# Kernel tuning notes

Hardware: AMD Instinct MI355X
Metric: run time of the kernel (lower is better)

## Reference

```python
import jax, jax.numpy as jnp
import numpy as np

D_MODEL = 1024


def setup_inputs() -> dict:
    key = jax.random.key(0)
    ks = jax.random.split(key, 7)
    s = 1.0 / np.sqrt(D_MODEL)
    return {
        "x": jax.random.normal(ks[0], (4, 4096, D_MODEL), dtype=jnp.float32),
        "Wq": jax.random.normal(ks[1], (D_MODEL, D_MODEL), dtype=jnp.float32) * s,
        "bq": jax.random.normal(ks[2], (D_MODEL,), dtype=jnp.float32) * s,
        "Wk": jax.random.normal(ks[3], (D_MODEL, D_MODEL), dtype=jnp.float32) * s,
        "bk": jax.random.normal(ks[4], (D_MODEL,), dtype=jnp.float32) * s,
        "Wv": jax.random.normal(ks[5], (D_MODEL, D_MODEL), dtype=jnp.float32) * s,
        "bv": jax.random.normal(ks[6], (D_MODEL,), dtype=jnp.float32) * s,
    }


def reference(x, Wq, bq, Wk, bk, Wv, bv):
    # nn.Linear: y = x @ W.T + b
    Q = jnp.einsum("bsd,ed->bse", x, Wq) + bq  # [B,S,D]
    K = jnp.einsum("bsd,ed->bse", x, Wk) + bk
    V = jnp.einsum("bsd,ed->bse", x, Wv) + bv
    scale = 1.0 / jnp.sqrt(jnp.asarray(x.shape[-1], dtype=x.dtype))
    KV = jnp.einsum("bsd,bse->bde", K, V) * scale  # [B,D,D]
    E = jnp.einsum("bsd,bde->bse", Q, KV)  # [B,S,D]
    return E
```

## Files before the change

### kernel.cpp

```cpp
#include <hip/hip_runtime.h>
#include <hip/hip_fp16.h>


#define BATCH 4
#define SEQ   4096
#define DM    1024

typedef _Float16 h8 __attribute__((ext_vector_type(8)));
typedef _Float16 h4 __attribute__((ext_vector_type(4)));
typedef float    f4 __attribute__((ext_vector_type(4)));

__device__ inline void gload_lds16(const _Float16* g, _Float16* l) {
    __builtin_amdgcn_global_load_lds(
        (const __attribute__((address_space(1))) void*)g,
        (__attribute__((address_space(3))) void*)l,
        16, 0, 0);
}

__device__ inline int xcd_swz(int bid, int grid) {
    const int q = grid >> 3;
    return (bid & 7) * q + (bid >> 3);
}

template<bool WRITE_RM>
__global__ __launch_bounds__(256) void cvt_transpose(
    const float* __restrict__ src, _Float16* __restrict__ dstT,
    _Float16* __restrict__ dstRM, int R, int C)
{
    __shared__ float tile[64][65];
    const long zoff = (long)blockIdx.z * R * C;
    src += zoff; dstT += zoff;
    if (WRITE_RM) dstRM += zoff;
    const int r0 = blockIdx.y * 64;
    const int c0 = blockIdx.x * 64;
    const int t  = threadIdx.x;
    const int tr = t >> 4;
    const int tc = (t & 15) * 4;
    #pragma unroll
    for (int i = 0; i < 4; ++i) {
        const int r = tr + i * 16;
        f4 v = *(const f4*)&src[(long)(r0 + r) * C + c0 + tc];
        tile[r][tc + 0] = v.x; tile[r][tc + 1] = v.y;
        tile[r][tc + 2] = v.z; tile[r][tc + 3] = v.w;
        if (WRITE_RM) {
            h4 h = { (_Float16)v.x, (_Float16)v.y, (_Float16)v.z, (_Float16)v.w };
            *(h4*)&dstRM[(long)(r0 + r) * C + c0 + tc] = h;
        }
    }
    __syncthreads();
    #pragma unroll
    for (int i = 0; i < 4; ++i) {
        const int c = tr + i * 16;
        h4 h = { (_Float16)tile[tc + 0][c], (_Float16)tile[tc + 1][c],
                 (_Float16)tile[tc + 2][c], (_Float16)tile[tc + 3][c] };
        *(h4*)&dstT[(long)(c0 + c) * R + r0 + tc] = h;
    }
}

__global__ __launch_bounds__(256) void cvt_pair(
    const float* __restrict__ s0, _Float16* __restrict__ d0,
    const float* __restrict__ s1, _Float16* __restrict__ d1)
{
    const int half = blockIdx.x >> 10;
    const long i = ((long)(blockIdx.x & 1023) * 256 + threadIdx.x) * 4;
    const float* s = half ? s1 : s0;
    _Float16*    d = half ? d1 : d0;
    f4 v = *(const f4*)(s + i);
    h4 h = { (_Float16)v.x, (_Float16)v.y, (_Float16)v.z, (_Float16)v.w };
    *(h4*)(d + i) = h;
}

__global__ __launch_bounds__(256) void rowsum_xt(
    const _Float16* __restrict__ xt, float* __restrict__ xs)
{
    const int gw   = blockIdx.x * 4 + (threadIdx.x >> 6);
    const int lane = threadIdx.x & 63;
    const _Float16* row = xt + (long)gw * SEQ;
    float s = 0.f;
    #pragma unroll
    for (int i = 0; i < SEQ; i += 512) {
        h8 v = *(const h8*)&row[i + lane * 8];
        #pragma unroll
        for (int j = 0; j < 8; ++j) s += (float)v[j];
    }
    #pragma unroll
    for (int off = 32; off; off >>= 1) s += __shfl_down(s, off);
    if (lane == 0) xs[gw] = s;
}

__global__ __launch_bounds__(256) void gemv_dual(
    const _Float16* __restrict__ Wvh, const _Float16* __restrict__ Wkh,
    const float* __restrict__ xs, const float* __restrict__ bv,
    float* __restrict__ dst)
{
    const int gw   = blockIdx.x * 4 + (threadIdx.x >> 6);
    const int half = gw >> 12;
    const int g    = gw & 4095;
    const int b    = g >> 10;
    const int o    = g & 1023;
    const int lane = threadIdx.x & 63;
    const _Float16* wr = (half ? Wkh : Wvh) + (long)o * 1024;
    const float*    v  = xs + b * 1024;
    float s = 0.f;
    #pragma unroll
    for (int i = 0; i < 2; ++i) {
        const int k = i * 512 + lane * 8;
        h8 wv = *(const h8*)&wr[k];
        f4 v0 = *(const f4*)&v[k];
        f4 v1 = *(const f4*)&v[k + 4];
        s += (float)wv[0] * v0.x + (float)wv[1] * v0.y +
             (float)wv[2] * v0.z + (float)wv[3] * v0.w +
             (float)wv[4] * v1.x + (float)wv[5] * v1.y +
             (float)wv[6] * v1.z + (float)wv[7] * v1.w;
    }
    #pragma unroll
    for (int off = 32; off; off >>= 1) s += __shfl_down(s, off);
    if (lane == 0) dst[gw] = s + (half ? 0.f : (float)SEQ * bv[o]);
}

__global__ __launch_bounds__(256) void gemv_k1024(
    const _Float16* __restrict__ W, long wZ,
    const float* __restrict__ vec, float* __restrict__ out)
{
    const int gw   = blockIdx.x * 4 + (threadIdx.x >> 6);
    const int b    = gw >> 10;
    const int o    = gw & 1023;
    const int lane = threadIdx.x & 63;
    const _Float16* wr = W + b * wZ + (long)o * 1024;
    float s = 0.f;
    #pragma unroll
    for (int i = 0; i < 2; ++i) {
        const int k = i * 512 + lane * 8;
        h8 wv = *(const h8*)&wr[k];
        f4 v0 = *(const f4*)&vec[k];
        f4 v1 = *(const f4*)&vec[k + 4];
        s += (float)wv[0] * v0.x + (float)wv[1] * v0.y +
             (float)wv[2] * v0.z + (float)wv[3] * v0.w +
             (float)wv[4] * v1.x + (float)wv[5] * v1.y +
             (float)wv[6] * v1.z + (float)wv[7] * v1.w;
    }
    #pragma unroll
    for (int off = 32; off; off >>= 1) s += __shfl_down(s, off);
    if (lane == 0) out[gw] = s;
}

__global__ __launch_bounds__(256) void reduce_gh(
    const _Float16* __restrict__ parts, _Float16* __restrict__ Gh)
{
    const long DD_ = (long)DM * DM;
    const long i = ((long)blockIdx.x * 256 + threadIdx.x) * 8;
    const long b = i >> 20;
    const long r = i & (DD_ - 1);
    const _Float16* p = parts + b * 4 * DD_ + r;
    h8 v0 = *(const h8*)&p[0];
    h8 v1 = *(const h8*)&p[DD_];
    h8 v2 = *(const h8*)&p[2 * DD_];
    h8 v3 = *(const h8*)&p[3 * DD_];
    h8 o;
    #pragma unroll
    for (int j = 0; j < 8; ++j) {
        float s = (float)v0[j] + (float)v1[j] + (float)v2[j] + (float)v3[j];
        o[j] = (_Float16)(s * 0.03125f);
    }
    *(h8*)&Gh[i] = o;
}

template<typename OutT, int BIAS>
__global__ __launch_bounds__(512, 1) void gemm8p(
    const _Float16* __restrict__ A, const _Float16* __restrict__ B,
    OutT* __restrict__ C,
    int K, int lda, int ldb, int ldc, int tilesX, int perZ,
    long aZ, long bZ, long cZ, int sk, long aK, long bK,
    const float* __restrict__ bc1, long bc1Z, float alpha)
{
    __shared__ _Float16 lds[2 * 32768];

    const int L  = xcd_swz(blockIdx.x, gridDim.x);
    const int z  = L / perZ;
    const int r0 = L - z * perZ;
    const int zb = z / sk;
    const int zk = z - zb * sk;
    A += (long)zb * aZ + (long)zk * aK;
    B += (long)zb * bZ + (long)zk * bK;
    C += (long)z * cZ;
    const float* pc1 = (BIAS == 1) ? bc1 + (long)zb * bc1Z : nullptr;

    const int tileM = (r0 / tilesX) * 256;
    const int tileN = (r0 % tilesX) * 256;
    const int tid   = threadIdx.x;
    const int lane  = tid & 63;
    const int wave  = tid >> 6;
    const int wr    = wave >> 2;
    const int wc    = wave & 3;
    const int la    = lane & 15;
    const int kg    = lane >> 4;

    auto stageA = [&](int buf, int mq, int kt) {
        _Float16* dst = &lds[buf * 32768 + mq * 8192];
        const int k0 = kt * 64;
        #pragma unroll
        for (int i = 0; i < 2; ++i) {
            const int U = i * 512 + tid;
            const int R = U >> 3, s = U & 7;
            const int gr = tileM + (R >> 6) * 128 + mq * 64 + (R & 63);
            gload_lds16(&A[(long)gr * lda + k0 + ((s ^ (R & 7)) << 3)], dst + U * 8);
        }
    };
    auto stageB = [&](int buf, int nq, int kt) {
        _Float16* dst = &lds[buf * 32768 + 16384 + nq * 8192];
        const int k0 = kt * 64;
        #pragma unroll
        for (int i = 0; i < 2; ++i) {
            const int U = i * 512 + tid;
            const int R = U >> 3, s = U & 7;
            const int gn = tileN + (R >> 5) * 64 + nq * 32 + (R & 31);
            gload_lds16(&B[(long)gn * ldb + k0 + ((s ^ (R & 7)) << 3)], dst + U * 8);
        }
    };

    f4 acc[8][4] = {};
    h8 af[4][2];
    h8 bf[2][2][2];

    auto readA = [&](int buf, int mq) {
        const _Float16* Ab = &lds[buf * 32768 + mq * 8192];
        #pragma unroll
        for (int mi = 0; mi < 4; ++mi)
            #pragma unroll
            for (int kk = 0; kk < 2; ++kk) {
                const int R = wr * 64 + mi * 16 + la;
                const int s = kk * 4 + kg;
                af[mi][kk] = *(const h8*)&Ab[R * 64 + ((s ^ (R & 7)) << 3)];
            }
    };
    auto readB = [&](int buf, int nq) {
        const _Float16* Bb = &lds[buf * 32768 + 16384 + nq * 8192];
        #pragma unroll
        for (int ni = 0; ni < 2; ++ni)
            #pragma unroll
            for (int kk = 0; kk < 2; ++kk) {
                const int R = wc * 32 + ni * 16 + la;
                const int s = kk * 4 + kg;
                bf[nq][ni][kk] = *(const h8*)&Bb[R * 64 + ((s ^ (R & 7)) << 3)];
            }
    };
    auto mfmaQ = [&](int mq, int nq) {
        __builtin_amdgcn_s_setprio(1);
        #pragma unroll
        for (int mi = 0; mi < 4; ++mi)
            #pragma unroll
            for (int ni = 0; ni < 2; ++ni)
                #pragma unroll
                for (int kk = 0; kk < 2; ++kk)
                    acc[mq * 4 + mi][nq * 2 + ni] =
                        __builtin_amdgcn_mfma_f32_16x16x32_f16(
                            af[mi][kk], bf[nq][ni][kk],
                            acc[mq * 4 + mi][nq * 2 + ni], 0, 0, 0);
        __builtin_amdgcn_s_setprio(0);
    };

    const int NT = K >> 6;

    stageA(0, 0, 0); stageA(0, 1, 0); stageB(0, 0, 0); stageB(0, 1, 0);
    if (NT > 1) {
        stageA(1, 0, 1); stageB(1, 0, 1);
        asm volatile("s_waitcnt vmcnt(4)" ::: "memory");
    } else {
        asm volatile("s_waitcnt vmcnt(0)" ::: "memory");
    }
    __builtin_amdgcn_sched_barrier(0);
    __builtin_amdgcn_s_barrier();

    for (int j = 0; j < NT; ++j) {
        const int buf = j & 1;
        readA(buf, 0); readB(buf, 0);
        if (j + 1 < NT) stageA(buf ^ 1, 1, j + 1);
        __builtin_amdgcn_s_barrier();
        mfmaQ(0, 0);
        __builtin_amdgcn_s_barrier();
        readB(buf, 1);
        if (j + 1 < NT) stageB(buf ^ 1, 1, j + 1);
        __builtin_amdgcn_s_barrier();
        mfmaQ(0, 1);
        __builtin_amdgcn_s_barrier();
        readA(buf, 1);
        if (j + 2 < NT) stageA(buf, 0, j + 2);
        __builtin_amdgcn_s_barrier();
        mfmaQ(1, 0);
        __builtin_amdgcn_s_barrier();
        if (j + 2 < NT) stageB(buf, 0, j + 2);
        __builtin_amdgcn_s_barrier();
        mfmaQ(1, 1);
        if (j + 2 < NT) {
            asm volatile("s_waitcnt vmcnt(4)" ::: "memory");
        } else if (j + 1 < NT) {
            asm volatile("s_waitcnt vmcnt(0)" ::: "memory");
        }
        __builtin_amdgcn_sched_barrier(0);
        __builtin_amdgcn_s_barrier();
    }

    #pragma unroll
    for (int mf = 0; mf < 8; ++mf) {
        #pragma unroll
        for (int nf = 0; nf < 4; ++nf) {
            const int col = tileN + wc * 64 + nf * 16 + la;
            #pragma unroll
            for (int jj = 0; jj < 4; ++jj) {
                const int row = tileM + wr * 128 + mf * 16 + kg * 4 + jj;
                float v = acc[mf][nf][jj] * alpha;
                if (BIAS == 1) v += pc1[col];
                C[(long)row * ldc + col] = (OutT)v;
            }
        }
    }
}

template<int BIAS>
__global__ __launch_bounds__(256) void gemm64(
    const _Float16* __restrict__ A, const _Float16* __restrict__ B,
    _Float16* __restrict__ C,
    int K, int lda, int ldb, int ldc, int tilesX, int perZ,
    long aZ, long bZ, long cZ,
    const float* __restrict__ bc1, long bc1Z,
    const float* __restrict__ br1, long br1Z,
    const float* __restrict__ bc2, long bc2Z,
    const float* __restrict__ br2, long br2Z,
    float beta)
{
    __shared__ _Float16 As[64 * 64];
    __shared__ _Float16 Bs[64 * 64];

    const int L  = xcd_swz(blockIdx.x, gridDim.x);
    const int z  = L / perZ;
    const int r0 = L - z * perZ;
    A += (long)z * aZ;
    B += (long)z * bZ;
    C += (long)z * cZ;
    const float* pc1 = nullptr; const float* pr1 = nullptr;
    const float* pc2 = nullptr; const float* pr2 = nullptr;
    if (BIAS == 3) {
        pc1 = bc1 + (long)z * bc1Z; pr1 = br1 + (long)z * br1Z;
        pc2 = bc2 + (long)z * bc2Z; pr2 = br2 + (long)z * br2Z;
    }

    const int tileM = (r0 / tilesX) * 64;
    const int tileN = (r0 % tilesX) * 64;
    const int tid   = threadIdx.x;
    const int lane  = tid & 63;
    const int wave  = tid >> 6;
    const int wm    = (wave >> 1) * 32;
    const int wn    = (wave & 1) * 32;
    const int srow  = tid >> 3;
    const int sslot = tid & 7;

    f4 acc[2][2] = {};
    const int arow = lane & 15;
    const int kg   = lane >> 4;

    for (int k0 = 0; k0 < K; k0 += 64) {
        #pragma unroll
        for (int i = 0; i < 2; ++i) {
            const int row   = i * 32 + srow;
            const int gslot = sslot ^ (row & 7);
            gload_lds16(&A[(long)(tileM + row) * lda + k0 + gslot * 8],
                        &As[row * 64 + sslot * 8]);
            gload_lds16(&B[(long)(tileN + row) * ldb + k0 + gslot * 8],
                        &Bs[row * 64 + sslot * 8]);
        }
        __syncthreads();

        #pragma unroll
        for (int kk = 0; kk < 64; kk += 32) {
            h8 af[2], bf[2];
            #pragma unroll
            for (int m = 0; m < 2; ++m) {
                const int rr   = wm + m * 16 + arow;
                const int slot = (kk >> 3) + kg;
                af[m] = *(const h8*)&As[rr * 64 + ((slot ^ (rr & 7)) << 3)];
            }
            #pragma unroll
            for (int n = 0; n < 2; ++n) {
                const int rr   = wn + n * 16 + arow;
                const int slot = (kk >> 3) + kg;
                bf[n] = *(const h8*)&Bs[rr * 64 + ((slot ^ (rr & 7)) << 3)];
            }
            #pragma unroll
            for (int m = 0; m < 2; ++m)
                #pragma unroll
                for (int n = 0; n < 2; ++n)
                    acc[m][n] = __builtin_amdgcn_mfma_f32_16x16x32_f16(
                        af[m], bf[n], acc[m][n], 0, 0, 0);
        }
        __syncthreads();
    }

    #pragma unroll
    for (int m = 0; m < 2; ++m) {
        #pragma unroll
        for (int n = 0; n < 2; ++n) {
            const int col = tileN + wn + n * 16 + arow;
            #pragma unroll
            for (int j = 0; j < 4; ++j) {
                const int row = tileM + wm + m * 16 + (lane >> 4) * 4 + j;
                float v = acc[m][n][j];
                if (BIAS == 3) v += beta * (pc1[col] * pr1[row] + pc2[col] * pr2[row]);
                C[(long)row * ldc + col] = (_Float16)v;
            }
        }
    }
}

extern "C" void kernel_launch(void* const* d_in, const int* in_sizes, int n_in,
                              void* d_out, int out_size, void* d_ws, size_t ws_size,
                              hipStream_t stream)
{
    const float* x  = (const float*)d_in[0];
    const float* Wq = (const float*)d_in[1];
    const float* bq = (const float*)d_in[2];
    const float* Wk = (const float*)d_in[3];
    const float* bk = (const float*)d_in[4];
    const float* Wv = (const float*)d_in[5];
    const float* bv = (const float*)d_in[6];
    float* out = (float*)d_out;

    const long DD = (long)DM * DM;
    const long DS = (long)DM * SEQ;

    char* base = (char*)d_ws;
    _Float16* xh   = (_Float16*)base;
    _Float16* xt   = (_Float16*)(base + 32l * 1024 * 1024);
    _Float16* Gh   = xt;
    _Float16* Ph   = xt + 4l * 1024 * 1024;
    _Float16* KVth = xt + 8l * 1024 * 1024;
    _Float16* Rth  = xt + 12l * 1024 * 1024;
    _Float16* Wqt  = (_Float16*)(base + 64l * 1024 * 1024);
    _Float16* Wkh  = Wqt + DD;
    _Float16* Wvh  = Wkh + DD;
    float*    xs   = (float*)(Wvh + DD);
    float*    u2   = xs + 4 * 1024;
    float*    w    = u2 + 4 * 1024;
    float*    cv   = w + 4 * 1024;
    _Float16* parts = (_Float16*)d_out;

    cvt_transpose<true ><<<dim3(16, 64, 4), 256, 0, stream>>>(x,  xt,  xh, SEQ, DM);
    cvt_transpose<false><<<dim3(16, 16, 1), 256, 0, stream>>>(Wq, Wqt, nullptr, DM, DM);
    cvt_pair<<<2048, 256, 0, stream>>>(Wk, Wkh, Wv, Wvh);

    rowsum_xt<<<1024, 256, 0, stream>>>(xt, xs);

    gemv_dual<<<2048, 256, 0, stream>>>(Wvh, Wkh, xs, bv, u2);

    gemm8p<_Float16, 0><<<256, 512, 0, stream>>>(
        xt, xt, parts, 1024, SEQ, SEQ, DM, 4, 16,
        DS, DS, DD, 4, 1024, 1024, nullptr, 0, 1.0f);

    reduce_gh<<<2048, 256, 0, stream>>>(parts, Gh);

    gemm64<0><<<1024, 256, 0, stream>>>(
        Wvh, Gh, Ph, 1024, DM, DM, DM, 16, 256,
        0, DD, DD, nullptr, 0, nullptr, 0, nullptr, 0, nullptr, 0, 0.f);

    gemm64<3><<<1024, 256, 0, stream>>>(
        Ph, Wkh, KVth, 1024, DM, DM, DM, 16, 256,
        DD, 0, DD, bk, 0, u2, 1024, w, 1024, bv, 0, 0.03125f);

    gemv_k1024<<<1024, 256, 0, stream>>>(KVth, DD, bq, cv);

    gemm64<0><<<1024, 256, 0, stream>>>(
        KVth, Wqt, Rth, 1024, DM, DM, DM, 16, 256,
        DD, 0, DD, nullptr, 0, nullptr, 0, nullptr, 0, nullptr, 0, 0.f);

    gemm8p<float, 1><<<256, 512, 0, stream>>>(
        xh, Rth, out, 1024, DM, DM, DM, 4, 64,
        DS, DD, DS, 1, 0, 0, cv, 1024, 1.0f);
}
```

Before: 174.2 us.

## Restructure gemm8p main loop into double-buffered register fragments with deeper prefetch

Rewrites the 256x256 GEMM main loop to process two K-tiles per iteration. It ping-pongs A and B fragments between two register sets so that each LDS read overlaps the previous quadrant's MFMAs, and it keeps both LDS buffers fully prefetched with a vmcnt(6) wait. This aims to hide LDS read latency behind MFMA work. The cost is higher register pressure, and the loop assumes NT is even (clamped stage indices re-load the last tile).

```diff
diff --git a/kernel.cpp b/kernel.cpp
--- a/kernel.cpp
+++ b/kernel.cpp
@@ -173,7 +173,7 @@
     long aZ, long bZ, long cZ, int sk, long aK, long bK,
     const float* __restrict__ bc1, long bc1Z, float alpha)
 {
-    __shared__ _Float16 lds[2 * 32768];
+    __shared__ _Float16 lds[2][4][8192];
 
     const int L  = xcd_swz(blockIdx.x, gridDim.x);
     const int z  = L / perZ;
@@ -194,9 +194,10 @@
     const int wc    = wave & 3;
     const int la    = lane & 15;
     const int kg    = lane >> 4;
+    const int NT    = K >> 6;
 
     auto stageA = [&](int buf, int mq, int kt) {
-        _Float16* dst = &lds[buf * 32768 + mq * 8192];
+        _Float16* dst = &lds[buf][mq][0];
         const int k0 = kt * 64;
         #pragma unroll
         for (int i = 0; i < 2; ++i) {
@@ -207,7 +208,7 @@
         }
     };
     auto stageB = [&](int buf, int nq, int kt) {
-        _Float16* dst = &lds[buf * 32768 + 16384 + nq * 8192];
+        _Float16* dst = &lds[buf][2 + nq][0];
         const int k0 = kt * 64;
         #pragma unroll
         for (int i = 0; i < 2; ++i) {
@@ -219,32 +220,32 @@
     };
 
     f4 acc[8][4] = {};
-    h8 af[4][2];
-    h8 bf[2][2][2];
-
-    auto readA = [&](int buf, int mq) {
-        const _Float16* Ab = &lds[buf * 32768 + mq * 8192];
+    h8 aS0[4][2], aS1[4][2];
+    h8 bS0[2][2], bS1[2][2];
+
+    auto readA = [&](h8 (*dst)[2], int buf, int mq) {
+        const _Float16* Ab = &lds[buf][mq][0];
         #pragma unroll
         for (int mi = 0; mi < 4; ++mi)
             #pragma unroll
             for (int kk = 0; kk < 2; ++kk) {
                 const int R = wr * 64 + mi * 16 + la;
                 const int s = kk * 4 + kg;
-                af[mi][kk] = *(const h8*)&Ab[R * 64 + ((s ^ (R & 7)) << 3)];
+                dst[mi][kk] = *(const h8*)&Ab[R * 64 + ((s ^ (R & 7)) << 3)];
             }
     };
-    auto readB = [&](int buf, int nq) {
-        const _Float16* Bb = &lds[buf * 32768 + 16384 + nq * 8192];
+    auto readB = [&](h8 (*dst)[2], int buf, int nq) {
+        const _Float16* Bb = &lds[buf][2 + nq][0];
         #pragma unroll
         for (int ni = 0; ni < 2; ++ni)
             #pragma unroll
             for (int kk = 0; kk < 2; ++kk) {
                 const int R = wc * 32 + ni * 16 + la;
                 const int s = kk * 4 + kg;
-                bf[nq][ni][kk] = *(const h8*)&Bb[R * 64 + ((s ^ (R & 7)) << 3)];
+                dst[ni][kk] = *(const h8*)&Bb[R * 64 + ((s ^ (R & 7)) << 3)];
             }
     };
-    auto mfmaQ = [&](int mq, int nq) {
+    auto mfmaQ = [&](int mq, int nq, h8 (*Af)[2], h8 (*Bf)[2]) {
         __builtin_amdgcn_s_setprio(1);
         #pragma unroll
         for (int mi = 0; mi < 4; ++mi)
@@ -254,48 +255,68 @@
                 for (int kk = 0; kk < 2; ++kk)
                     acc[mq * 4 + mi][nq * 2 + ni] =
                         __builtin_amdgcn_mfma_f32_16x16x32_f16(
-                            af[mi][kk], bf[nq][ni][kk],
+                            Af[mi][kk], Bf[ni][kk],
                             acc[mq * 4 + mi][nq * 2 + ni], 0, 0, 0);
         __builtin_amdgcn_s_setprio(0);
     };
 
-    const int NT = K >> 6;
-
     stageA(0, 0, 0); stageA(0, 1, 0); stageB(0, 0, 0); stageB(0, 1, 0);
-    if (NT > 1) {
-        stageA(1, 0, 1); stageB(1, 0, 1);
-        asm volatile("s_waitcnt vmcnt(4)" ::: "memory");
-    } else {
-        asm volatile("s_waitcnt vmcnt(0)" ::: "memory");
-    }
+    stageA(1, 0, 1); stageA(1, 1, 1); stageB(1, 0, 1); stageB(1, 1, 1);
+    asm volatile("s_waitcnt vmcnt(8)" ::: "memory");
     __builtin_amdgcn_sched_barrier(0);
     __builtin_amdgcn_s_barrier();
-
-    for (int j = 0; j < NT; ++j) {
-        const int buf = j & 1;
-        readA(buf, 0); readB(buf, 0);
-        if (j + 1 < NT) stageA(buf ^ 1, 1, j + 1);
-        __builtin_amdgcn_s_barrier();
-        mfmaQ(0, 0);
-        __builtin_amdgcn_s_barrier();
-        readB(buf, 1);
-        if (j + 1 < NT) stageB(buf ^ 1, 1, j + 1);
-        __builtin_amdgcn_s_barrier();
-        mfmaQ(0, 1);
-        __builtin_amdgcn_s_barrier();
-        readA(buf, 1);
-        if (j + 2 < NT) stageA(buf, 0, j + 2);
-        __builtin_amdgcn_s_barrier();
-        mfmaQ(1, 0);
-        __builtin_amdgcn_s_barrier();
-        if (j + 2 < NT) stageB(buf, 0, j + 2);
-        __builtin_amdgcn_s_barrier();
-        mfmaQ(1, 1);
-        if (j + 2 < NT) {
-            asm volatile("s_waitcnt vmcnt(4)" ::: "memory");
-        } else if (j + 1 < NT) {
-            asm volatile("s_waitcnt vmcnt(0)" ::: "memory");
-        }
+    readA(aS0, 0, 0);
+    readB(bS0, 0, 0);
+    asm volatile("s_waitcnt lgkmcnt(0)" ::: "memory");
+    __builtin_amdgcn_sched_barrier(0);
+    __builtin_amdgcn_s_barrier();
+
+    for (int i = 0; i < NT / 2; ++i) {
+        const int t  = 2 * i;
+        const int t2 = (t + 2 < NT) ? t + 2 : NT - 1;
+        const int t3 = (t + 3 < NT) ? t + 3 : NT - 1;
+        readB(bS1, 0, 1);
+        stageA(0, 0, t2);
+        __builtin_amdgcn_s_barrier();
+        mfmaQ(0, 0, aS0, bS0);
+        __builtin_amdgcn_s_barrier();
+        readA(aS1, 0, 1);
+        stageB(0, 0, t2);
+        __builtin_amdgcn_s_barrier();
+        mfmaQ(0, 1, aS0, bS1);
+        __builtin_amdgcn_s_barrier();
+        readA(aS0, 1, 0);
+        stageB(0, 1, t2);
+        __builtin_amdgcn_s_barrier();
+        mfmaQ(1, 0, aS1, bS0);
+        __builtin_amdgcn_s_barrier();
+        readB(bS0, 1, 0);
+        stageA(0, 1, t2);
+        __builtin_amdgcn_s_barrier();
+        mfmaQ(1, 1, aS1, bS1);
+        asm volatile("s_waitcnt vmcnt(6)" ::: "memory");
+        __builtin_amdgcn_sched_barrier(0);
+        __builtin_amdgcn_s_barrier();
+        readB(bS1, 1, 1);
+        stageA(1, 0, t3);
+        __builtin_amdgcn_s_barrier();
+        mfmaQ(0, 0, aS0, bS0);
+        __builtin_amdgcn_s_barrier();
+        readA(aS1, 1, 1);
+        stageB(1, 0, t3);
+        __builtin_amdgcn_s_barrier();
+        mfmaQ(0, 1, aS0, bS1);
+        __builtin_amdgcn_s_barrier();
+        readA(aS0, 0, 0);
+        stageB(1, 1, t3);
+        __builtin_amdgcn_s_barrier();
+        mfmaQ(1, 0, aS1, bS0);
+        __builtin_amdgcn_s_barrier();
+        readB(bS0, 0, 0);
+        stageA(1, 1, t3);
+        __builtin_amdgcn_s_barrier();
+        mfmaQ(1, 1, aS1, bS1);
+        asm volatile("s_waitcnt vmcnt(6)" ::: "memory");
         __builtin_amdgcn_sched_barrier(0);
         __builtin_amdgcn_s_barrier();
     }
@@ -448,7 +469,6 @@
     cvt_pair<<<2048, 256, 0, stream>>>(Wk, Wkh, Wv, Wvh);
 
     rowsum_xt<<<1024, 256, 0, stream>>>(xt, xs);
-
     gemv_dual<<<2048, 256, 0, stream>>>(Wvh, Wkh, xs, bv, u2);
 
     gemm8p<_Float16, 0><<<256, 512, 0, stream>>>(
```

After: 196.8 us. +13.0%, slower.

## Reassociate weight products to drop one batched GEMM from the chain

Applied to the files above, without the earlier changes.

Precomputes the batch-independent product Wk·Wq (Mh) inside the same launch as the P = Wv·G GEMM. The separate KV GEMM and the KV·Wq GEMM are replaced by a single GEMM of P against Mh, with bias terms folded into extra GEMV vectors (qk, qw, sv, cv). Weight conversion kernels are merged into one launch, and LDS wait counts are made explicit around the MFMA phases of gemm8p. The aim is to remove one 1024³×4 GEMM and several launches, at the cost of extra GEMVs and a different fp16 rounding order.

```diff
diff --git a/kernel.cpp b/kernel.cpp
--- a/kernel.cpp
+++ b/kernel.cpp
@@ -22,85 +22,7 @@
     return (bid & 7) * q + (bid >> 3);
 }
 
-template<bool WRITE_RM>
-__global__ __launch_bounds__(256) void cvt_transpose(
-    const float* __restrict__ src, _Float16* __restrict__ dstT,
-    _Float16* __restrict__ dstRM, int R, int C)
-{
-    __shared__ float tile[64][65];
-    const long zoff = (long)blockIdx.z * R * C;
-    src += zoff; dstT += zoff;
-    if (WRITE_RM) dstRM += zoff;
-    const int r0 = blockIdx.y * 64;
-    const int c0 = blockIdx.x * 64;
-    const int t  = threadIdx.x;
-    const int tr = t >> 4;
-    const int tc = (t & 15) * 4;
-    #pragma unroll
-    for (int i = 0; i < 4; ++i) {
-        const int r = tr + i * 16;
-        f4 v = *(const f4*)&src[(long)(r0 + r) * C + c0 + tc];
-        tile[r][tc + 0] = v.x; tile[r][tc + 1] = v.y;
-        tile[r][tc + 2] = v.z; tile[r][tc + 3] = v.w;
-        if (WRITE_RM) {
-            h4 h = { (_Float16)v.x, (_Float16)v.y, (_Float16)v.z, (_Float16)v.w };
-            *(h4*)&dstRM[(long)(r0 + r) * C + c0 + tc] = h;
-        }
-    }
-    __syncthreads();
-    #pragma unroll
-    for (int i = 0; i < 4; ++i) {
-        const int c = tr + i * 16;
-        h4 h = { (_Float16)tile[tc + 0][c], (_Float16)tile[tc + 1][c],
-                 (_Float16)tile[tc + 2][c], (_Float16)tile[tc + 3][c] };
-        *(h4*)&dstT[(long)(c0 + c) * R + r0 + tc] = h;
-    }
-}
-
-__global__ __launch_bounds__(256) void cvt_pair(
-    const float* __restrict__ s0, _Float16* __restrict__ d0,
-    const float* __restrict__ s1, _Float16* __restrict__ d1)
-{
-    const int half = blockIdx.x >> 10;
-    const long i = ((long)(blockIdx.x & 1023) * 256 + threadIdx.x) * 4;
-    const float* s = half ? s1 : s0;
-    _Float16*    d = half ? d1 : d0;
-    f4 v = *(const f4*)(s + i);
-    h4 h = { (_Float16)v.x, (_Float16)v.y, (_Float16)v.z, (_Float16)v.w };
-    *(h4*)(d + i) = h;
-}
-
-__global__ __launch_bounds__(256) void rowsum_xt(
-    const _Float16* __restrict__ xt, float* __restrict__ xs)
-{
-    const int gw   = blockIdx.x * 4 + (threadIdx.x >> 6);
-    const int lane = threadIdx.x & 63;
-    const _Float16* row = xt + (long)gw * SEQ;
-    float s = 0.f;
-    #pragma unroll
-    for (int i = 0; i < SEQ; i += 512) {
-        h8 v = *(const h8*)&row[i + lane * 8];
-        #pragma unroll
-        for (int j = 0; j < 8; ++j) s += (float)v[j];
-    }
-    #pragma unroll
-    for (int off = 32; off; off >>= 1) s += __shfl_down(s, off);
-    if (lane == 0) xs[gw] = s;
-}
-
-__global__ __launch_bounds__(256) void gemv_dual(
-    const _Float16* __restrict__ Wvh, const _Float16* __restrict__ Wkh,
-    const float* __restrict__ xs, const float* __restrict__ bv,
-    float* __restrict__ dst)
-{
-    const int gw   = blockIdx.x * 4 + (threadIdx.x >> 6);
-    const int half = gw >> 12;
-    const int g    = gw & 4095;
-    const int b    = g >> 10;
-    const int o    = g & 1023;
-    const int lane = threadIdx.x & 63;
-    const _Float16* wr = (half ? Wkh : Wvh) + (long)o * 1024;
-    const float*    v  = xs + b * 1024;
+__device__ inline float doth(const _Float16* wr, const float* v, int lane) {
     float s = 0.f;
     #pragma unroll
     for (int i = 0; i < 2; ++i) {
@@ -113,35 +35,165 @@
              (float)wv[4] * v1.x + (float)wv[5] * v1.y +
              (float)wv[6] * v1.z + (float)wv[7] * v1.w;
     }
+    return s;
+}
+__device__ inline float dotf(const float* a, const float* b, int lane) {
+    float s = 0.f;
+    #pragma unroll
+    for (int i = 0; i < 4; ++i) {
+        const int k = i * 256 + lane * 4;
+        f4 x = *(const f4*)&a[k];
+        f4 y = *(const f4*)&b[k];
+        s += x.x * y.x + x.y * y.y + x.z * y.z + x.w * y.w;
+    }
+    return s;
+}
+__device__ inline float wred(float s) {
     #pragma unroll
     for (int off = 32; off; off >>= 1) s += __shfl_down(s, off);
-    if (lane == 0) dst[gw] = s + (half ? 0.f : (float)SEQ * bv[o]);
-}
-
-__global__ __launch_bounds__(256) void gemv_k1024(
-    const _Float16* __restrict__ W, long wZ,
-    const float* __restrict__ vec, float* __restrict__ out)
+    return s;
+}
+
+__global__ __launch_bounds__(256) void cvt_x(
+    const float* __restrict__ src, _Float16* __restrict__ dstT,
+    _Float16* __restrict__ dstRM, int R, int C)
+{
+    __shared__ float tile[64][65];
+    const long zoff = (long)blockIdx.z * R * C;
+    src += zoff; dstT += zoff; dstRM += zoff;
+    const int r0 = blockIdx.y * 64;
+    const int c0 = blockIdx.x * 64;
+    const int t  = threadIdx.x;
+    const int tr = t >> 4;
+    const int tc = (t & 15) * 4;
+    #pragma unroll
+    for (int i = 0; i < 4; ++i) {
+        const int r = tr + i * 16;
+        f4 v = *(const f4*)&src[(long)(r0 + r) * C + c0 + tc];
+        tile[r][tc + 0] = v.x; tile[r][tc + 1] = v.y;
+        tile[r][tc + 2] = v.z; tile[r][tc + 3] = v.w;
+        h4 h = { (_Float16)v.x, (_Float16)v.y, (_Float16)v.z, (_Float16)v.w };
+        *(h4*)&dstRM[(long)(r0 + r) * C + c0 + tc] = h;
+    }
+    __syncthreads();
+    #pragma unroll
+    for (int i = 0; i < 4; ++i) {
+        const int c = tr + i * 16;
+        h4 h = { (_Float16)tile[tc + 0][c], (_Float16)tile[tc + 1][c],
+                 (_Float16)tile[tc + 2][c], (_Float16)tile[tc + 3][c] };
+        *(h4*)&dstT[(long)(c0 + c) * R + r0 + tc] = h;
+    }
+}
+
+__global__ __launch_bounds__(256) void wcvt(
+    const float* __restrict__ Wq, const float* __restrict__ Wk,
+    const float* __restrict__ Wv,
+    _Float16* __restrict__ Wqt, _Float16* __restrict__ Wkt,
+    _Float16* __restrict__ Wkh, _Float16* __restrict__ Wvh)
+{
+    __shared__ float tile[64][65];
+    const int z = blockIdx.z;
+    const float* src = z == 0 ? Wq : (z == 1 ? Wk : Wv);
+    _Float16* dstT  = z == 0 ? Wqt : (z == 1 ? Wkt : nullptr);
+    _Float16* dstRM = z == 0 ? nullptr : (z == 1 ? Wkh : Wvh);
+    const int r0 = blockIdx.y * 64;
+    const int c0 = blockIdx.x * 64;
+    const int t  = threadIdx.x;
+    const int tr = t >> 4;
+    const int tc = (t & 15) * 4;
+    #pragma unroll
+    for (int i = 0; i < 4; ++i) {
+        const int r = tr + i * 16;
+        f4 v = *(const f4*)&src[(long)(r0 + r) * DM + c0 + tc];
+        tile[r][tc + 0] = v.x; tile[r][tc + 1] = v.y;
+        tile[r][tc + 2] = v.z; tile[r][tc + 3] = v.w;
+        if (dstRM) {
+            h4 h = { (_Float16)v.x, (_Float16)v.y, (_Float16)v.z, (_Float16)v.w };
+            *(h4*)&dstRM[(long)(r0 + r) * DM + c0 + tc] = h;
+        }
+    }
+    __syncthreads();
+    if (dstT) {
+        #pragma unroll
+        for (int i = 0; i < 4; ++i) {
+            const int c = tr + i * 16;
+            h4 h = { (_Float16)tile[tc + 0][c], (_Float16)tile[tc + 1][c],
+                     (_Float16)tile[tc + 2][c], (_Float16)tile[tc + 3][c] };
+            *(h4*)&dstT[(long)(c0 + c) * DM + r0 + tc] = h;
+        }
+    }
+}
+
+__global__ __launch_bounds__(256) void rowsum_xt(
+    const _Float16* __restrict__ xt, float* __restrict__ xs)
 {
     const int gw   = blockIdx.x * 4 + (threadIdx.x >> 6);
+    const int lane = threadIdx.x & 63;
+    const _Float16* row = xt + (long)gw * SEQ;
+    float s = 0.f;
+    #pragma unroll
+    for (int i = 0; i < SEQ; i += 512) {
+        h8 v = *(const h8*)&row[i + lane * 8];
+        #pragma unroll
+        for (int j = 0; j < 8; ++j) s += (float)v[j];
+    }
+    s = wred(s);
+    if (lane == 0) xs[gw] = s;
+}
+
+__global__ __launch_bounds__(256) void gemv_misc(
+    const _Float16* __restrict__ Wvh, const _Float16* __restrict__ Wkh,
+    const _Float16* __restrict__ Wqt, const _Float16* __restrict__ Wkt,
+    const float* __restrict__ xs, const float* __restrict__ bv,
+    const float* __restrict__ bk, const float* __restrict__ bq,
+    float* __restrict__ vecs)
+{
+    const int gw   = blockIdx.x * 4 + (threadIdx.x >> 6);
+    const int lane = threadIdx.x & 63;
+    const _Float16* wr;
+    const float* v;
+    if (gw < 4096)      { wr = Wvh + (long)(gw & 1023) * DM; v = xs + (gw >> 10) * DM; }
+    else if (gw < 8192) { wr = Wkh + (long)(gw & 1023) * DM; v = xs + ((gw - 4096) >> 10) * DM; }
+    else if (gw < 9216) { wr = Wqt + (long)(gw - 8192) * DM; v = bk; }
+    else                { wr = Wkt + (long)(gw - 9216) * DM; v = bq; }
+    float s = wred(doth(wr, v, lane));
+    if (lane == 0) {
+        if (gw < 4096) s += (float)SEQ * bv[gw & 1023];
+        vecs[gw] = s;
+    }
+}
+
+__global__ __launch_bounds__(256) void gemv_qw(
+    const _Float16* __restrict__ Wqt, const float* __restrict__ w,
+    const float* __restrict__ bq, const float* __restrict__ bk,
+    float* __restrict__ qw, float* __restrict__ sv)
+{
+    const int gw   = blockIdx.x * 4 + (threadIdx.x >> 6);
+    const int lane = threadIdx.x & 63;
+    if (gw < 4096) {
+        float s = wred(doth(Wqt + (long)(gw & 1023) * DM, w + (gw >> 10) * DM, lane));
+        if (lane == 0) qw[gw] = s;
+    } else if (gw == 4096) {
+        float s = wred(dotf(bq, bk, lane));
+        if (lane == 0) sv[0] = s;
+    } else if (gw <= 4100) {
+        float s = wred(dotf(bq, w + (gw - 4097) * DM, lane));
+        if (lane == 0) sv[1 + (gw - 4097)] = s;
+    }
+}
+
+__global__ __launch_bounds__(256) void gemv_cv(
+    const _Float16* __restrict__ Ph, const float* __restrict__ kb,
+    const float* __restrict__ u2, const float* __restrict__ bv,
+    const float* __restrict__ sv, float* __restrict__ cv)
+{
+    const int gw   = blockIdx.x * 4 + (threadIdx.x >> 6);
+    const int lane = threadIdx.x & 63;
     const int b    = gw >> 10;
-    const int o    = gw & 1023;
-    const int lane = threadIdx.x & 63;
-    const _Float16* wr = W + b * wZ + (long)o * 1024;
-    float s = 0.f;
-    #pragma unroll
-    for (int i = 0; i < 2; ++i) {
-        const int k = i * 512 + lane * 8;
-        h8 wv = *(const h8*)&wr[k];
-        f4 v0 = *(const f4*)&vec[k];
-        f4 v1 = *(const f4*)&vec[k + 4];
-        s += (float)wv[0] * v0.x + (float)wv[1] * v0.y +
-             (float)wv[2] * v0.z + (float)wv[3] * v0.w +
-             (float)wv[4] * v1.x + (float)wv[5] * v1.y +
-             (float)wv[6] * v1.z + (float)wv[7] * v1.w;
-    }
-    #pragma unroll
-    for (int off = 32; off; off >>= 1) s += __shfl_down(s, off);
-    if (lane == 0) out[gw] = s;
+    const int e    = gw & 1023;
+    float s = wred(doth(Ph + (long)b * DM * DM + (long)e * DM, kb, lane));
+    if (lane == 0)
+        cv[gw] = s + (sv[0] * u2[gw] + sv[1 + b] * bv[e]) * 0.03125f;
 }
 
 __global__ __launch_bounds__(256) void reduce_gh(
@@ -275,17 +327,24 @@
         const int buf = j & 1;
         readA(buf, 0); readB(buf, 0);
         if (j + 1 < NT) stageA(buf ^ 1, 1, j + 1);
-        __builtin_amdgcn_s_barrier();
+        asm volatile("s_waitcnt lgkmcnt(8)" ::: "memory");
+        __builtin_amdgcn_s_barrier();
+        asm volatile("s_waitcnt lgkmcnt(0)" ::: "memory");
+        __builtin_amdgcn_sched_barrier(0);
         mfmaQ(0, 0);
         __builtin_amdgcn_s_barrier();
         readB(buf, 1);
         if (j + 1 < NT) stageB(buf ^ 1, 1, j + 1);
         __builtin_amdgcn_s_barrier();
+        asm volatile("s_waitcnt lgkmcnt(0)" ::: "memory");
+        __builtin_amdgcn_sched_barrier(0);
         mfmaQ(0, 1);
         __builtin_amdgcn_s_barrier();
         readA(buf, 1);
         if (j + 2 < NT) stageA(buf, 0, j + 2);
         __builtin_amdgcn_s_barrier();
+        asm volatile("s_waitcnt lgkmcnt(0)" ::: "memory");
+        __builtin_amdgcn_sched_barrier(0);
         mfmaQ(1, 0);
         __builtin_amdgcn_s_barrier();
         if (j + 2 < NT) stageB(buf, 0, j + 2);
@@ -320,20 +379,23 @@
 __global__ __launch_bounds__(256) void gemm64(
     const _Float16* __restrict__ A, const _Float16* __restrict__ B,
     _Float16* __restrict__ C,
+    const _Float16* __restrict__ A2, const _Float16* __restrict__ B2,
+    _Float16* __restrict__ C2, int zSplit,
     int K, int lda, int ldb, int ldc, int tilesX, int perZ,
     long aZ, long bZ, long cZ,
     const float* __restrict__ bc1, long bc1Z,
     const float* __restrict__ br1, long br1Z,
     const float* __restrict__ bc2, long bc2Z,
     const float* __restrict__ br2, long br2Z,
-    float beta)
+    float alpha, float beta)
 {
     __shared__ _Float16 As[64 * 64];
     __shared__ _Float16 Bs[64 * 64];
 
     const int L  = xcd_swz(blockIdx.x, gridDim.x);
-    const int z  = L / perZ;
+    int z        = L / perZ;
     const int r0 = L - z * perZ;
+    if (z >= zSplit) { A = A2; B = B2; C = C2; z = 0; }
     A += (long)z * aZ;
     B += (long)z * bZ;
     C += (long)z * cZ;
@@ -403,7 +465,7 @@
             #pragma unroll
             for (int j = 0; j < 4; ++j) {
                 const int row = tileM + wm + m * 16 + (lane >> 4) * 4 + j;
-                float v = acc[m][n][j];
+                float v = acc[m][n][j] * alpha;
                 if (BIAS == 3) v += beta * (pc1[col] * pr1[row] + pc2[col] * pr2[row]);
                 C[(long)row * ldc + col] = (_Float16)v;
             }
@@ -426,30 +488,38 @@
 
     const long DD = (long)DM * DM;
     const long DS = (long)DM * SEQ;
+    const long MB = 1024l * 1024;
 
     char* base = (char*)d_ws;
     _Float16* xh   = (_Float16*)base;
-    _Float16* xt   = (_Float16*)(base + 32l * 1024 * 1024);
+    _Float16* xt   = (_Float16*)(base + 32 * MB);
     _Float16* Gh   = xt;
-    _Float16* Ph   = xt + 4l * 1024 * 1024;
-    _Float16* KVth = xt + 8l * 1024 * 1024;
-    _Float16* Rth  = xt + 12l * 1024 * 1024;
-    _Float16* Wqt  = (_Float16*)(base + 64l * 1024 * 1024);
-    _Float16* Wkh  = Wqt + DD;
-    _Float16* Wvh  = Wkh + DD;
-    float*    xs   = (float*)(Wvh + DD);
-    float*    u2   = xs + 4 * 1024;
-    float*    w    = u2 + 4 * 1024;
-    float*    cv   = w + 4 * 1024;
+    _Float16* Ph   = (_Float16*)(base + 40 * MB);
+    _Float16* Rth  = (_Float16*)(base + 48 * MB);
+    _Float16* Wqt  = (_Float16*)(base + 64 * MB);
+    _Float16* Wkh  = (_Float16*)(base + 66 * MB);
+    _Float16* Wvh  = (_Float16*)(base + 68 * MB);
+    _Float16* Wkt  = (_Float16*)(base + 70 * MB);
+    _Float16* Mh   = (_Float16*)(base + 72 * MB);
+    float*    vecs = (float*)(base + 74 * MB);
+    float*    u2   = vecs;
+    float*    w    = vecs + 4096;
+    float*    qk   = vecs + 8192;
+    float*    kb   = vecs + 9216;
+    float*    xs   = vecs + 10240;
+    float*    qw   = vecs + 14336;
+    float*    cv   = vecs + 18432;
+    float*    sv   = vecs + 22528;
     _Float16* parts = (_Float16*)d_out;
 
-    cvt_transpose<true ><<<dim3(16, 64, 4), 256, 0, stream>>>(x,  xt,  xh, SEQ, DM);
-    cvt_transpose<false><<<dim3(16, 16, 1), 256, 0, stream>>>(Wq, Wqt, nullptr, DM, DM);
-    cvt_pair<<<2048, 256, 0, stream>>>(Wk, Wkh, Wv, Wvh);
+    cvt_x<<<dim3(16, 64, 4), 256, 0, stream>>>(x, xt, xh, SEQ, DM);
+    wcvt<<<dim3(16, 16, 3), 256, 0, stream>>>(Wq, Wk, Wv, Wqt, Wkt, Wkh, Wvh);
 
     rowsum_xt<<<1024, 256, 0, stream>>>(xt, xs);
 
-    gemv_dual<<<2048, 256, 0, stream>>>(Wvh, Wkh, xs, bv, u2);
+    gemv_misc<<<2560, 256, 0, stream>>>(Wvh, Wkh, Wqt, Wkt, xs, bv, bk, bq, vecs);
+
+    gemv_qw<<<1026, 256, 0, stream>>>(Wqt, w, bq, bk, qw, sv);
 
     gemm8p<_Float16, 0><<<256, 512, 0, stream>>>(
         xt, xt, parts, 1024, SEQ, SEQ, DM, 4, 16,
@@ -457,19 +527,19 @@
 
     reduce_gh<<<2048, 256, 0, stream>>>(parts, Gh);
 
-    gemm64<0><<<1024, 256, 0, stream>>>(
-        Wvh, Gh, Ph, 1024, DM, DM, DM, 16, 256,
-        0, DD, DD, nullptr, 0, nullptr, 0, nullptr, 0, nullptr, 0, 0.f);
+    gemm64<0><<<1280, 256, 0, stream>>>(
+        Wvh, Gh, Ph, Wqt, Wkt, Mh, 4,
+        1024, DM, DM, DM, 16, 256,
+        0, DD, DD,
+        nullptr, 0, nullptr, 0, nullptr, 0, nullptr, 0, 1.0f, 0.f);
+
+    gemv_cv<<<1024, 256, 0, stream>>>(Ph, kb, u2, bv, sv, cv);
 
     gemm64<3><<<1024, 256, 0, stream>>>(
-        Ph, Wkh, KVth, 1024, DM, DM, DM, 16, 256,
-        DD, 0, DD, bk, 0, u2, 1024, w, 1024, bv, 0, 0.03125f);
-
-    gemv_k1024<<<1024, 256, 0, stream>>>(KVth, DD, bq, cv);
-
-    gemm64<0><<<1024, 256, 0, stream>>>(
-        KVth, Wqt, Rth, 1024, DM, DM, DM, 16, 256,
-        DD, 0, DD, nullptr, 0, nullptr, 0, nullptr, 0, nullptr, 0, 0.f);
+        Ph, Mh, Rth, nullptr, nullptr, nullptr, 99,
+        1024, DM, DM, DM, 16, 256,
+        DD, 0, DD,
+        qk, 0, u2, 1024, qw, 1024, bv, 0, 1.0f, 0.03125f);
 
     gemm8p<float, 1><<<256, 512, 0, stream>>>(
         xh, Rth, out, 1024, DM, DM, DM, 4, 64,
```

New measurement: 168.1 us. 3.5% less time.
